# Optimization experiments

Measured on AMD Instinct MI355X. Metric: run time of the kernel, lower is better.

## Reference

```python
import jax, jax.numpy as jnp
import numpy as np

B, T_HIST, T_OUT, T_FC = 4096, 168, 48, 49
N_LABELS, F_CTL, F_FC, HID = 64, 16, 8, 32
EPS = 1e-7


def setup_inputs() -> dict:
    key = jax.random.key(0)
    ks = jax.random.split(key, 18)
    rn = lambda k, s, sc=1.0: jax.random.normal(k, s, jnp.float32) * sc
    return {
        "history": rn(ks[0], (B, T_HIST, N_LABELS)),
        "control": rn(ks[1], (B, T_OUT, F_CTL)),
        "forecasts": rn(ks[2], (B, T_FC, F_FC)),
        "h_mean": rn(ks[3], (N_LABELS,), 0.1),
        "h_var": jax.random.uniform(ks[4], (N_LABELS,), jnp.float32, 0.5, 1.5),
        "c_mean": rn(ks[5], (F_CTL,), 0.1),
        "c_var": jax.random.uniform(ks[6], (F_CTL,), jnp.float32, 0.5, 1.5),
        "f_mean": rn(ks[7], (), 0.1),
        "f_var": jax.random.uniform(ks[8], (), jnp.float32, 0.5, 1.5),
        "conv_w": rn(ks[9], (2, F_FC, 4), 0.2),   # kernel_size=2, Conv1D(4)
        "conv_b": rn(ks[10], (4,), 0.01),
        "lstm_k": rn(ks[11], (N_LABELS, 4 * HID), 0.1),
        "lstm_rk": rn(ks[12], (HID, 4 * HID), 0.1),
        "lstm_b": rn(ks[13], (4 * HID,), 0.01),
        "w1": rn(ks[14], (HID + F_CTL + 4, 64), 0.1),
        "b1": rn(ks[15], (64,), 0.01),
        "w2": rn(ks[16], (64, N_LABELS), 0.05),
        "b2": rn(ks[17], (N_LABELS,), 0.01),
    }


def _norm(x, m, v):
    # keras Normalization: (x - mean) / max(sqrt(var), eps)
    return (x - m) / jnp.maximum(jnp.sqrt(v), EPS)


def _lstm(x, h, c, k, rk, b):
    z = x @ k + h @ rk + b                      # [B, 4*HID], gate order i,f,g,o
    i, f, g, o = jnp.split(z, 4, axis=-1)
    c2 = jax.nn.sigmoid(f) * c + jax.nn.sigmoid(i) * jnp.tanh(g)
    h2 = jax.nn.sigmoid(o) * jnp.tanh(c2)
    return h2, c2


def _mlp(x1, x2, x3, w1, b1, w2, b2):
    x = jnp.concatenate([x1, x2, x3], axis=-1)  # [B, 52]
    return jax.nn.relu(x @ w1 + b1) @ w2 + b2


def reference(history, control, forecasts, h_mean, h_var, c_mean, c_var,
              f_mean, f_var, conv_w, conv_b, lstm_k, lstm_rk, lstm_b,
              w1, b1, w2, b2):
    latest = history[:, -1, :]                               # [B, N_LABELS]
    cn = _norm(control, c_mean, c_var)                       # [B, T_OUT, F_CTL]
    fn = _norm(forecasts, f_mean, f_var)                     # scalar norm
    # Conv1D(filters=4, kernel_size=2), valid padding -> [B, T_FC-1, 4]
    fc = fn[:, :-1] @ conv_w[0] + fn[:, 1:] @ conv_w[1] + conv_b

    # encoder LSTM over normalized history
    hn = _norm(history, h_mean, h_var)
    bsz = history.shape[0]
    init = (jnp.zeros((bsz, HID), hn.dtype), jnp.zeros((bsz, HID), hn.dtype))

    def enc_step(carry, x):
        h, c = carry
        return _lstm(x, h, c, lstm_k, lstm_rk, lstm_b), None

    (h, c), _ = jax.lax.scan(enc_step, init, jnp.swapaxes(hn, 0, 1))

    # pre-loop step (its prediction write is overwritten by loop i=0, but it
    # updates `latest` which feeds the loop)
    latest = latest + _mlp(h, cn[:, 0], fc[:, 0], w1, b1, w2, b2)

    t_out = control.shape[1]

    def dec_step(carry, inp):
        latest, h, c = carry
        ctl, fci = inp
        xn = _norm(latest, h_mean, h_var)
        h2, c2 = _lstm(xn, h, c, lstm_k, lstm_rk, lstm_b)
        latest2 = latest + _mlp(h2, ctl, fci, w1, b1, w2, b2)
        return (latest2, h2, c2), latest2

    xs = (jnp.swapaxes(cn, 0, 1), jnp.swapaxes(fc[:, :t_out], 0, 1))
    _, preds = jax.lax.scan(dec_step, (latest, h, c), xs)   # [T_OUT, B, N]
    return jnp.swapaxes(preds, 0, 1)                        # [B, T_OUT, N]
```

## Files before the change

### kernel.cpp

```cpp
#include <hip/hip_runtime.h>

#define EPSV 1e-7f

typedef __bf16 bf16x8 __attribute__((ext_vector_type(8)));
typedef float  f32x4  __attribute__((ext_vector_type(4)));
typedef unsigned int   u32x4 __attribute__((ext_vector_type(4)));
typedef unsigned short u16x8 __attribute__((ext_vector_type(8)));
typedef unsigned short u16x4 __attribute__((ext_vector_type(4)));

__device__ __forceinline__ unsigned short f2bf(float f) {
    unsigned int u = __float_as_uint(f);
    return (unsigned short)((u + 0x7FFFu + ((u >> 16) & 1u)) >> 16);
}
__device__ __forceinline__ float bf2f(unsigned short u) {
    return __uint_as_float(((unsigned int)u) << 16);
}
__device__ __forceinline__ void split2(float f, unsigned short& hi, unsigned short& lo) {
    hi = f2bf(f);
    lo = f2bf(f - bf2f(hi));
}
__device__ __forceinline__ void splitT(float f, unsigned short& hi, unsigned short& lo) {
    unsigned int u  = __float_as_uint(f);
    unsigned int hb = u & 0xFFFF0000u;
    float l = f - __uint_as_float(hb);
    hi = (unsigned short)(u >> 16);
    lo = (unsigned short)(__float_as_uint(l) >> 16);
}
__device__ __forceinline__ float sigf(float x) {
    return __builtin_amdgcn_rcpf(1.0f + __expf(-x));
}
__device__ __forceinline__ float tanhfast(float x) {
    float cx = fminf(fmaxf(x, -15.0f), 15.0f);
    float e = __expf(2.0f * cx);
    return (e - 1.0f) * __builtin_amdgcn_rcpf(e + 1.0f);
}
__device__ __forceinline__ float xor8(float v) {
    return __builtin_bit_cast(float, __builtin_amdgcn_update_dpp(
        0, __builtin_bit_cast(int, v), 0x128, 0xF, 0xF, true));
}

#define MFMA16(A, B, C) __builtin_amdgcn_mfma_f32_16x16x32_bf16(A, B, C, 0, 0, 0)
#define BC8(x) __builtin_bit_cast(bf16x8, x)

#define BARRIER() do {                                        \
    asm volatile("s_waitcnt lgkmcnt(0)" ::: "memory");        \
    __builtin_amdgcn_s_barrier();                             \
    __builtin_amdgcn_sched_barrier(0);                        \
} while (0)

#define HS2 72
#define MS  136
#define XS2 136

__global__ __launch_bounds__(256) void tutina_kernel(
    const float* __restrict__ history, const float* __restrict__ control,
    const float* __restrict__ forecasts,
    const float* __restrict__ h_mean, const float* __restrict__ h_var,
    const float* __restrict__ c_mean, const float* __restrict__ c_var,
    const float* __restrict__ f_mean, const float* __restrict__ f_var,
    const float* __restrict__ conv_w, const float* __restrict__ conv_b,
    const float* __restrict__ lstm_k, const float* __restrict__ lstm_rk,
    const float* __restrict__ lstm_b,
    const float* __restrict__ w1, const float* __restrict__ b1,
    const float* __restrict__ w2, const float* __restrict__ b2,
    float* __restrict__ out)
{
    __shared__ unsigned short hbuf[2][16 * HS2];
    __shared__ unsigned short xbuf[16 * XS2];
    __shared__ unsigned short mlps[16 * MS];
    __shared__ unsigned short hids[16 * MS];
    __shared__ unsigned int   fcs[48 * 64];

    const int tid  = threadIdx.x;
    const int lane = tid & 63;
    const int wid  = tid >> 6;
    const int l15  = lane & 15;
    const int l4   = lane >> 4;
    const int b0   = blockIdx.x * 16;

    for (int i = tid; i < 16 * HS2; i += 256) hbuf[0][i] = 0;
    for (int i = tid; i < 16 * MS;  i += 256) mlps[i] = 0;

    const int  uu     = l15 & 7;
    const bool lohalf = (l15 < 8);
    const int  u      = wid * 8 + uu;
    const int  jz0    = lohalf ? u      : 32 + u;
    const int  jz1    = lohalf ? 64 + u : 96 + u;
    const int  j1     = wid * 16 + l15;

    auto bfragK = [&](int kbase, int j, float& dacc, bf16x8& H, bf16x8& L) {
        u16x8 h, l;
#pragma unroll
        for (int i = 0; i < 8; i++) {
            int k = kbase + l4 * 8 + i;
            float sv = 1.0f / fmaxf(sqrtf(h_var[k]), EPSV);
            float w  = lstm_k[k * 128 + j] * sv;
            dacc += h_mean[k] * w;
            unsigned short hh, ll; split2(w, hh, ll);
            h[i] = hh; l[i] = ll;
        }
        H = BC8(h); L = BC8(l);
    };
    auto bfragP = [&](const float* W, int ldw, int kbase, int j, bf16x8& H, bf16x8& L) {
        u16x8 h, l;
#pragma unroll
        for (int i = 0; i < 8; i++) {
            int k = kbase + l4 * 8 + i;
            float w = W[k * ldw + j];
            unsigned short hh, ll; split2(w, hh, ll);
            h[i] = hh; l[i] = ll;
        }
        H = BC8(h); L = BC8(l);
    };
    auto bfragW11 = [&](int j, float& dacc, bf16x8& H, bf16x8& L) {
        u16x8 h, l;
#pragma unroll
        for (int i = 0; i < 8; i++) {
            int k = 32 + l4 * 8 + i;
            float w = 0.0f;
            if (k < 52) {
                w = w1[k * 64 + j];
                if (k < 48) {
                    float sv = 1.0f / fmaxf(sqrtf(c_var[k - 32]), EPSV);
                    w *= sv;
                    dacc += c_mean[k - 32] * w;
                }
            }
            unsigned short hh, ll; split2(w, hh, ll);
            h[i] = hh; l[i] = ll;
        }
        H = BC8(h); L = BC8(l);
    };

    bf16x8 fA0h, fA0l, fA1h, fA1l, fA2h, fA2l;
    bf16x8 fB0h, fB0l, fB1h, fB1l, fB2h, fB2l;
    bf16x8 fW10h, fW10l, fW11h, fW11l, fW20h, fW20l, fW21h, fW21l;
    float dz0 = 0.f, dz1 = 0.f, d1 = 0.f;
    bfragK(0,  jz0, dz0, fA0h, fA0l);
    bfragK(32, jz0, dz0, fA1h, fA1l);
    bfragP(lstm_rk, 128, 0, jz0, fA2h, fA2l);
    bfragK(0,  jz1, dz1, fB0h, fB0l);
    bfragK(32, jz1, dz1, fB1h, fB1l);
    bfragP(lstm_rk, 128, 0, jz1, fB2h, fB2l);
    bfragP(w1, 64, 0, j1, fW10h, fW10l);
    bfragW11(j1, d1, fW11h, fW11l);
    bfragP(w2, 64, 0,  j1, fW20h, fW20l);
    bfragP(w2, 64, 32, j1, fW21h, fW21l);

    dz0 += __shfl_xor(dz0, 16, 64); dz0 += __shfl_xor(dz0, 32, 64);
    dz1 += __shfl_xor(dz1, 16, 64); dz1 += __shfl_xor(dz1, 32, 64);
    d1  += __shfl_xor(d1, 16, 64);  d1  += __shfl_xor(d1, 32, 64);
    float pd0 = xor8(dz0), pd1 = xor8(dz1);
    const float bi_ = lstm_b[u]      - (lohalf ? dz0 : pd0);
    const float bf_ = lstm_b[32 + u] - (lohalf ? pd0 : dz0);
    const float bg_ = lstm_b[64 + u] - (lohalf ? dz1 : pd1);
    const float bo_ = lstm_b[96 + u] - (lohalf ? pd1 : dz1);
    const float b1j = b1[j1] - d1;
    const float b2j = b2[j1];

    const int r0 = l4 * 4 + (lohalf ? 0 : 2);
    const int r1 = r0 + 1;
    float c0 = 0.0f, c1 = 0.0f;

    const int rc = tid >> 2, cc = (tid & 3) * 4;

    {
        float fm  = f_mean[0];
        float fsc = 1.0f / fmaxf(sqrtf(f_var[0]), EPSV);
        for (int cell = tid; cell < 48 * 64; cell += 256) {
            int t  = cell >> 6;
            int b  = (cell >> 2) & 15;
            int uc = cell & 3;
            const float* fp = forecasts + ((size_t)(b0 + b) * 49 + t) * 8;
            float acc = conv_b[uc];
#pragma unroll
            for (int k = 0; k < 8; k++) {
                acc += (fp[k]     - fm) * fsc * conv_w[k * 4 + uc];
                acc += (fp[8 + k] - fm) * fsc * conv_w[32 + k * 4 + uc];
            }
            unsigned short hh, ll; split2(acc, hh, ll);
            fcs[cell] = ((unsigned int)hh << 16) | ll;
        }
    }

    auto lstm_gates = [&](const f32x4& a, const f32x4& b,
                          unsigned short* hw, bool write_mlp) {
        float sa0 = lohalf ? a[2] : a[0];
        float sa1 = lohalf ? a[3] : a[1];
        float sb0 = lohalf ? b[2] : b[0];
        float sb1 = lohalf ? b[3] : b[1];
        float ra0 = xor8(sa0);
        float ra1 = xor8(sa1);
        float rb0 = xor8(sb0);
        float rb1 = xor8(sb1);
        float zi0 = (lohalf ? a[0] : ra0) + bi_;
        float zi1 = (lohalf ? a[1] : ra1) + bi_;
        float zf0 = (lohalf ? ra0 : a[2]) + bf_;
        float zf1 = (lohalf ? ra1 : a[3]) + bf_;
        float zg0 = (lohalf ? b[0] : rb0) + bg_;
        float zg1 = (lohalf ? b[1] : rb1) + bg_;
        float zo0 = (lohalf ? rb0 : b[2]) + bo_;
        float zo1 = (lohalf ? rb1 : b[3]) + bo_;
        c0 = sigf(zf0) * c0 + sigf(zi0) * tanhfast(zg0);
        c1 = sigf(zf1) * c1 + sigf(zi1) * tanhfast(zg1);
        float h20 = sigf(zo0) * tanhfast(c0);
        float h21 = sigf(zo1) * tanhfast(c1);
        unsigned short bh, bl;
        splitT(h20, bh, bl);
        hw[r0 * HS2 + u]      = bh;
        hw[r0 * HS2 + 32 + u] = bl;
        if (write_mlp) { mlps[r0 * MS + u] = bh; mlps[r0 * MS + 64 + u] = bl; }
        splitT(h21, bh, bl);
        hw[r1 * HS2 + u]      = bh;
        hw[r1 * HS2 + 32 + u] = bl;
        if (write_mlp) { mlps[r1 * MS + u] = bh; mlps[r1 * MS + 64 + u] = bl; }
    };

    const float* hp = history + (size_t)(b0 + l15) * (168 * 64);
    const int o1 = l4 * 8, o2 = 32 + l4 * 8;

    auto mk_frags = [&](const f32x4& p0, const f32x4& p1, const f32x4& p2,
                        const f32x4& p3, bf16x8& A0h, bf16x8& A0l,
                        bf16x8& A1h, bf16x8& A1l) {
        u16x8 xh_, xl_;
        unsigned short hh, ll;
#pragma unroll
        for (int i = 0; i < 4; i++) { splitT(p0[i], hh, ll); xh_[i] = hh; xl_[i] = ll; }
#pragma unroll
        for (int i = 0; i < 4; i++) { splitT(p1[i], hh, ll); xh_[4+i] = hh; xl_[4+i] = ll; }
        A0h = BC8(xh_); A0l = BC8(xl_);
#pragma unroll
        for (int i = 0; i < 4; i++) { splitT(p2[i], hh, ll); xh_[i] = hh; xl_[i] = ll; }
#pragma unroll
        for (int i = 0; i < 4; i++) { splitT(p3[i], hh, ll); xh_[4+i] = hh; xl_[4+i] = ll; }
        A1h = BC8(xh_); A1l = BC8(xl_);
    };
    auto zx12 = [&](bf16x8 A0h, bf16x8 A0l, bf16x8 A1h, bf16x8 A1l,
                    f32x4& zn0, f32x4& zn1) {
        f32x4 s0 = {0.f,0.f,0.f,0.f}, s1 = {0.f,0.f,0.f,0.f};
        s0 = MFMA16(A0h, fA0h, s0);  s1 = MFMA16(A0h, fB0h, s1);
        s0 = MFMA16(A1h, fA1h, s0);  s1 = MFMA16(A1h, fB1h, s1);
        s0 = MFMA16(A0l, fA0h, s0);  s1 = MFMA16(A0l, fB0h, s1);
        s0 = MFMA16(A1l, fA1h, s0);  s1 = MFMA16(A1l, fB1h, s1);
        s0 = MFMA16(A0h, fA0l, s0);  s1 = MFMA16(A0h, fB0l, s1);
        s0 = MFMA16(A1h, fA1l, s0);  s1 = MFMA16(A1h, fB1l, s1);
        zn0 = s0; zn1 = s1;
    };

    f32x4 zx0, zx1;
    {
        f32x4 p0 = *(const f32x4*)(hp + o1), p1 = *(const f32x4*)(hp + o1 + 4);
        f32x4 p2 = *(const f32x4*)(hp + o2), p3 = *(const f32x4*)(hp + o2 + 4);
        bf16x8 A0h, A0l, A1h, A1l;
        mk_frags(p0, p1, p2, p3, A0h, A0l, A1h, A1l);
        zx12(A0h, A0l, A1h, A1l, zx0, zx1);
    }
    f32x4 vb0 = *(const f32x4*)(hp + 64 + o1), vb1 = *(const f32x4*)(hp + 64 + o1 + 4);
    f32x4 vb2 = *(const f32x4*)(hp + 64 + o2), vb3 = *(const f32x4*)(hp + 64 + o2 + 4);

    BARRIER();

    for (int t = 0; t < 168; ++t) {
        const int p = t & 1;
        const unsigned short* hr = hbuf[p];
        bf16x8 a2h = BC8(*(const u32x4*)&hr[l15 * HS2 + l4 * 8]);
        bf16x8 a2l = BC8(*(const u32x4*)&hr[l15 * HS2 + 32 + l4 * 8]);

        bf16x8 A0h, A0l, A1h, A1l;
        mk_frags(vb0, vb1, vb2, vb3, A0h, A0l, A1h, A1l);
        const float* np = hp + (size_t)((t < 166) ? t + 2 : 167) * 64;
        vb0 = *(const f32x4*)(np + o1); vb1 = *(const f32x4*)(np + o1 + 4);
        vb2 = *(const f32x4*)(np + o2); vb3 = *(const f32x4*)(np + o2 + 4);

        f32x4 zn0, zn1;
        zx12(A0h, A0l, A1h, A1l, zn0, zn1);

        f32x4 z0 = zx0, z1 = zx1;
        z0 = MFMA16(a2h, fA2h, z0);  z1 = MFMA16(a2h, fB2h, z1);
        z0 = MFMA16(a2l, fA2h, z0);  z1 = MFMA16(a2l, fB2h, z1);
        z0 = MFMA16(a2h, fA2l, z0);  z1 = MFMA16(a2h, fB2l, z1);

        lstm_gates(z0, z1, hbuf[p ^ 1], t == 167);
        BARRIER();
        zx0 = zn0; zx1 = zn1;
    }

    float lat0 = history[((size_t)(b0 + l4 * 4 + 0) * 168 + 167) * 64 + j1];
    float lat1 = history[((size_t)(b0 + l4 * 4 + 1) * 168 + 167) * 64 + j1];
    float lat2 = history[((size_t)(b0 + l4 * 4 + 2) * 168 + 167) * 64 + j1];
    float lat3 = history[((size_t)(b0 + l4 * 4 + 3) * 168 + 167) * 64 + j1];
    f32x4 creg = {0.f, 0.f, 0.f, 0.f};
    if (tid < 64)
        creg = *(const f32x4*)(control + ((size_t)(b0 + rc) * 48 + 0) * 16 + cc);

    auto stage_cn = [&](const f32x4& v) {
        if (tid < 64) {
            u16x4 oh, ol;
#pragma unroll
            for (int q = 0; q < 4; q++) {
                unsigned short hh, ll;
                splitT(v[q], hh, ll);
                oh[q] = hh; ol[q] = ll;
            }
            *(u16x4*)&mlps[rc * MS + 32 + cc]      = oh;
            *(u16x4*)&mlps[rc * MS + 64 + 32 + cc] = ol;
        }
    };
    auto stage_fc = [&](int t) {
        if (tid >= 64 && tid < 128) {
            int q = tid - 64;
            unsigned int v = fcs[t * 64 + q];
            mlps[(q >> 2) * MS + 48 + (q & 3)]      = (unsigned short)(v >> 16);
            mlps[(q >> 2) * MS + 64 + 48 + (q & 3)] = (unsigned short)(v & 0xFFFFu);
        }
    };

    auto mlp1 = [&]() {
        const int mbase = l15 * MS + l4 * 8;
        bf16x8 m0  = BC8(*(const u32x4*)&mlps[mbase]);
        bf16x8 m1  = BC8(*(const u32x4*)&mlps[mbase + 32]);
        bf16x8 m0l = BC8(*(const u32x4*)&mlps[mbase + 64]);
        bf16x8 m1l = BC8(*(const u32x4*)&mlps[mbase + 96]);
        f32x4 ha = {0.f,0.f,0.f,0.f}, hb = {0.f,0.f,0.f,0.f};
        ha = MFMA16(m0,  fW10h, ha);   hb = MFMA16(m1,  fW11h, hb);
        ha = MFMA16(m0l, fW10h, ha);   hb = MFMA16(m1l, fW11h, hb);
        ha = MFMA16(m0,  fW10l, ha);   hb = MFMA16(m1,  fW11l, hb);
        f32x4 hacc = ha + hb;
#pragma unroll
        for (int q = 0; q < 4; q++) {
            float hv = fmaxf(hacc[q] + b1j, 0.0f);
            unsigned short hh, ll;
            splitT(hv, hh, ll);
            hids[(l4 * 4 + q) * MS + j1]      = hh;
            hids[(l4 * 4 + q) * MS + 64 + j1] = ll;
        }
    };
    auto mlp2 = [&]() {
        const int mbase = l15 * MS + l4 * 8;
        bf16x8 h0  = BC8(*(const u32x4*)&hids[mbase]);
        bf16x8 h1  = BC8(*(const u32x4*)&hids[mbase + 32]);
        bf16x8 h0l = BC8(*(const u32x4*)&hids[mbase + 64]);
        bf16x8 h1l = BC8(*(const u32x4*)&hids[mbase + 96]);
        f32x4 oa = {0.f,0.f,0.f,0.f}, ob = {0.f,0.f,0.f,0.f};
        oa = MFMA16(h0,  fW20h, oa);   ob = MFMA16(h1,  fW21h, ob);
        oa = MFMA16(h0l, fW20h, oa);   ob = MFMA16(h1l, fW21h, ob);
        oa = MFMA16(h0,  fW20l, oa);   ob = MFMA16(h1,  fW21l, ob);
        f32x4 oacc = oa + ob;
        lat0 += oacc[0] + b2j;
        lat1 += oacc[1] + b2j;
        lat2 += oacc[2] + b2j;
        lat3 += oacc[3] + b2j;
    };

    stage_cn(creg);
    stage_fc(0);
    BARRIER();
    mlp1();
    BARRIER();
    mlp2();

    for (int t = 0; t < 48; ++t) {
        const int p = t & 1;
        unsigned short bh, bl;
        splitT(lat0, bh, bl);
        xbuf[(l4 * 4 + 0) * XS2 + j1] = bh; xbuf[(l4 * 4 + 0) * XS2 + 64 + j1] = bl;
        splitT(lat1, bh, bl);
        xbuf[(l4 * 4 + 1) * XS2 + j1] = bh; xbuf[(l4 * 4 + 1) * XS2 + 64 + j1] = bl;
        splitT(lat2, bh, bl);
        xbuf[(l4 * 4 + 2) * XS2 + j1] = bh; xbuf[(l4 * 4 + 2) * XS2 + 64 + j1] = bl;
        splitT(lat3, bh, bl);
        xbuf[(l4 * 4 + 3) * XS2 + j1] = bh; xbuf[(l4 * 4 + 3) * XS2 + 64 + j1] = bl;
        stage_cn(creg);
        stage_fc(t);
        int tn = (t < 47) ? t + 1 : 47;
        if (tid < 64)
            creg = *(const f32x4*)(control + ((size_t)(b0 + rc) * 48 + tn) * 16 + cc);
        BARRIER();

        const unsigned short* hr = hbuf[p];
        const int xb = l15 * XS2 + l4 * 8;
        bf16x8 a0h = BC8(*(const u32x4*)&xbuf[xb]);
        bf16x8 a1h = BC8(*(const u32x4*)&xbuf[xb + 32]);
        bf16x8 a0l = BC8(*(const u32x4*)&xbuf[xb + 64]);
        bf16x8 a1l = BC8(*(const u32x4*)&xbuf[xb + 96]);
        bf16x8 a2h = BC8(*(const u32x4*)&hr[l15 * HS2 + l4 * 8]);
        bf16x8 a2l = BC8(*(const u32x4*)&hr[l15 * HS2 + 32 + l4 * 8]);
        f32x4 z0a = {0.f,0.f,0.f,0.f}, z0b = {0.f,0.f,0.f,0.f};
        f32x4 z1a = {0.f,0.f,0.f,0.f}, z1b = {0.f,0.f,0.f,0.f};
        z0a = MFMA16(a0h, fA0h, z0a);  z1a = MFMA16(a0h, fB0h, z1a);
        z0b = MFMA16(a1h, fA1h, z0b);  z1b = MFMA16(a1h, fB1h, z1b);
        z0a = MFMA16(a2h, fA2h, z0a);  z1a = MFMA16(a2h, fB2h, z1a);
        z0b = MFMA16(a0l, fA0h, z0b);  z1b = MFMA16(a0l, fB0h, z1b);
        z0a = MFMA16(a1l, fA1h, z0a);  z1a = MFMA16(a1l, fB1h, z1a);
        z0b = MFMA16(a2l, fA2h, z0b);  z1b = MFMA16(a2l, fB2h, z1b);
        z0a = MFMA16(a0h, fA0l, z0a);  z1a = MFMA16(a0h, fB0l, z1a);
        z0b = MFMA16(a1h, fA1l, z0b);  z1b = MFMA16(a1h, fB1l, z1b);
        z0a = MFMA16(a2h, fA2l, z0a);  z1a = MFMA16(a2h, fB2l, z1a);
        f32x4 z0 = z0a + z0b, z1 = z1a + z1b;
        lstm_gates(z0, z1, hbuf[p ^ 1], true);
        BARRIER();

        mlp1();
        BARRIER();
        mlp2();

        out[((size_t)(b0 + l4 * 4 + 0) * 48 + t) * 64 + j1] = lat0;
        out[((size_t)(b0 + l4 * 4 + 1) * 48 + t) * 64 + j1] = lat1;
        out[((size_t)(b0 + l4 * 4 + 2) * 48 + t) * 64 + j1] = lat2;
        out[((size_t)(b0 + l4 * 4 + 3) * 48 + t) * 64 + j1] = lat3;
    }
}

extern "C" void kernel_launch(void* const* d_in, const int* in_sizes, int n_in,
                              void* d_out, int out_size, void* d_ws, size_t ws_size,
                              hipStream_t stream) {
    tutina_kernel<<<dim3(256), dim3(256), 0, stream>>>(
        (const float*)d_in[0],  (const float*)d_in[1],  (const float*)d_in[2],
        (const float*)d_in[3],  (const float*)d_in[4],  (const float*)d_in[5],
        (const float*)d_in[6],  (const float*)d_in[7],  (const float*)d_in[8],
        (const float*)d_in[9],  (const float*)d_in[10], (const float*)d_in[11],
        (const float*)d_in[12], (const float*)d_in[13], (const float*)d_in[14],
        (const float*)d_in[15], (const float*)d_in[16], (const float*)d_in[17],
        (float*)d_out);
}
```

Measured before the change: 186.1 us.

## Split block into recurrent and producer wave groups to overlap encoder input projection

The block grows to 512 threads as two groups of four waves. Group A does only the recurrent h@rk MFMAs and gate math, at raised priority. Group B loads history, computes the input projection one step ahead into a double-buffered shared buffer, and handles the MLP in the decoder. The aim is to take the input-projection work and global loads off the serial critical path of the 168-step recurrence. The cost is twice the waves per block, extra shared memory, and idle waves in each group during the other's phases.

```diff
diff --git a/kernel.cpp b/kernel.cpp
--- a/kernel.cpp
+++ b/kernel.cpp
@@ -51,8 +51,9 @@
 #define HS2 72
 #define MS  136
 #define XS2 136
-
-__global__ __launch_bounds__(256) void tutina_kernel(
+#define ZS3 20
+
+__global__ __launch_bounds__(512, 1) void tutina_kernel(
     const float* __restrict__ history, const float* __restrict__ control,
     const float* __restrict__ forecasts,
     const float* __restrict__ h_mean, const float* __restrict__ h_var,
@@ -66,6 +67,7 @@
     float* __restrict__ out)
 {
     __shared__ unsigned short hbuf[2][16 * HS2];
+    __shared__ float zxb[2][4][2][16 * ZS3];
     __shared__ unsigned short xbuf[16 * XS2];
     __shared__ unsigned short mlps[16 * MS];
     __shared__ unsigned short hids[16 * MS];
@@ -74,19 +76,22 @@
     const int tid  = threadIdx.x;
     const int lane = tid & 63;
     const int wid  = tid >> 6;
+    const int wa   = wid & 3;
+    const bool gA  = (wid < 4);
+    const int lt   = tid & 255;
     const int l15  = lane & 15;
     const int l4   = lane >> 4;
     const int b0   = blockIdx.x * 16;
 
-    for (int i = tid; i < 16 * HS2; i += 256) hbuf[0][i] = 0;
-    for (int i = tid; i < 16 * MS;  i += 256) mlps[i] = 0;
+    for (int i = tid; i < 16 * HS2; i += 512) hbuf[0][i] = 0;
+    for (int i = tid; i < 16 * MS;  i += 512) mlps[i] = 0;
 
     const int  uu     = l15 & 7;
     const bool lohalf = (l15 < 8);
-    const int  u      = wid * 8 + uu;
+    const int  u      = wa * 8 + uu;
     const int  jz0    = lohalf ? u      : 32 + u;
     const int  jz1    = lohalf ? 64 + u : 96 + u;
-    const int  j1     = wid * 16 + l15;
+    const int  j1     = wa * 16 + l15;
 
     auto bfragK = [&](int kbase, int j, float& dacc, bf16x8& H, bf16x8& L) {
         u16x8 h, l;
@@ -132,42 +137,51 @@
         H = BC8(h); L = BC8(l);
     };
 
-    bf16x8 fA0h, fA0l, fA1h, fA1l, fA2h, fA2l;
-    bf16x8 fB0h, fB0l, fB1h, fB1l, fB2h, fB2l;
-    bf16x8 fW10h, fW10l, fW11h, fW11l, fW20h, fW20l, fW21h, fW21l;
-    float dz0 = 0.f, dz1 = 0.f, d1 = 0.f;
+    bf16x8 fA0h, fA0l, fA1h, fA1l, fB0h, fB0l, fB1h, fB1l;
+    float dz0 = 0.f, dz1 = 0.f;
     bfragK(0,  jz0, dz0, fA0h, fA0l);
     bfragK(32, jz0, dz0, fA1h, fA1l);
-    bfragP(lstm_rk, 128, 0, jz0, fA2h, fA2l);
     bfragK(0,  jz1, dz1, fB0h, fB0l);
     bfragK(32, jz1, dz1, fB1h, fB1l);
-    bfragP(lstm_rk, 128, 0, jz1, fB2h, fB2l);
-    bfragP(w1, 64, 0, j1, fW10h, fW10l);
-    bfragW11(j1, d1, fW11h, fW11l);
-    bfragP(w2, 64, 0,  j1, fW20h, fW20l);
-    bfragP(w2, 64, 32, j1, fW21h, fW21l);
-
-    dz0 += __shfl_xor(dz0, 16, 64); dz0 += __shfl_xor(dz0, 32, 64);
-    dz1 += __shfl_xor(dz1, 16, 64); dz1 += __shfl_xor(dz1, 32, 64);
-    d1  += __shfl_xor(d1, 16, 64);  d1  += __shfl_xor(d1, 32, 64);
-    float pd0 = xor8(dz0), pd1 = xor8(dz1);
-    const float bi_ = lstm_b[u]      - (lohalf ? dz0 : pd0);
-    const float bf_ = lstm_b[32 + u] - (lohalf ? pd0 : dz0);
-    const float bg_ = lstm_b[64 + u] - (lohalf ? dz1 : pd1);
-    const float bo_ = lstm_b[96 + u] - (lohalf ? pd1 : dz1);
-    const float b1j = b1[j1] - d1;
-    const float b2j = b2[j1];
-
-    const int r0 = l4 * 4 + (lohalf ? 0 : 2);
-    const int r1 = r0 + 1;
-    float c0 = 0.0f, c1 = 0.0f;
-
-    const int rc = tid >> 2, cc = (tid & 3) * 4;
-
-    {
+
+    bf16x8 fA2h, fA2l, fB2h, fB2l;
+    float bi_ = 0.f, bf_ = 0.f, bg_ = 0.f, bo_ = 0.f;
+    if (gA) {
+        bfragP(lstm_rk, 128, 0, jz0, fA2h, fA2l);
+        bfragP(lstm_rk, 128, 0, jz1, fB2h, fB2l);
+        float z0s = dz0, z1s = dz1;
+        z0s += __shfl_xor(z0s, 16, 64); z0s += __shfl_xor(z0s, 32, 64);
+        z1s += __shfl_xor(z1s, 16, 64); z1s += __shfl_xor(z1s, 32, 64);
+        float pd0 = xor8(z0s), pd1 = xor8(z1s);
+        bi_ = lstm_b[u]      - (lohalf ? z0s : pd0);
+        bf_ = lstm_b[32 + u] - (lohalf ? pd0 : z0s);
+        bg_ = lstm_b[64 + u] - (lohalf ? z1s : pd1);
+        bo_ = lstm_b[96 + u] - (lohalf ? pd1 : z1s);
+    }
+
+    bf16x8 fW10h, fW10l, fW11h, fW11l, fW20h, fW20l, fW21h, fW21l;
+    float b1j = 0.f, b2j = 0.f;
+    float lat0 = 0.f, lat1 = 0.f, lat2 = 0.f, lat3 = 0.f;
+    f32x4 creg = {0.f, 0.f, 0.f, 0.f};
+    const int rc = lt >> 2, cc = (lt & 3) * 4;
+    if (!gA) {
+        bfragP(w1, 64, 0, j1, fW10h, fW10l);
+        float d1 = 0.f;
+        bfragW11(j1, d1, fW11h, fW11l);
+        bfragP(w2, 64, 0,  j1, fW20h, fW20l);
+        bfragP(w2, 64, 32, j1, fW21h, fW21l);
+        d1 += __shfl_xor(d1, 16, 64); d1 += __shfl_xor(d1, 32, 64);
+        b1j = b1[j1] - d1;
+        b2j = b2[j1];
+        lat0 = history[((size_t)(b0 + l4 * 4 + 0) * 168 + 167) * 64 + j1];
+        lat1 = history[((size_t)(b0 + l4 * 4 + 1) * 168 + 167) * 64 + j1];
+        lat2 = history[((size_t)(b0 + l4 * 4 + 2) * 168 + 167) * 64 + j1];
+        lat3 = history[((size_t)(b0 + l4 * 4 + 3) * 168 + 167) * 64 + j1];
+        if (lt < 64)
+            creg = *(const f32x4*)(control + ((size_t)(b0 + rc) * 48 + 0) * 16 + cc);
         float fm  = f_mean[0];
         float fsc = 1.0f / fmaxf(sqrtf(f_var[0]), EPSV);
-        for (int cell = tid; cell < 48 * 64; cell += 256) {
+        for (int cell = lt; cell < 48 * 64; cell += 256) {
             int t  = cell >> 6;
             int b  = (cell >> 2) & 15;
             int uc = cell & 3;
@@ -182,6 +196,10 @@
             fcs[cell] = ((unsigned int)hh << 16) | ll;
         }
     }
+
+    const int r0 = l4 * 4 + (lohalf ? 0 : 2);
+    const int r1 = r0 + 1;
+    float c0 = 0.0f, c1 = 0.0f;
 
     auto lstm_gates = [&](const f32x4& a, const f32x4& b,
                           unsigned short* hw, bool write_mlp) {
@@ -216,9 +234,6 @@
         if (write_mlp) { mlps[r1 * MS + u] = bh; mlps[r1 * MS + 64 + u] = bl; }
     };
 
-    const float* hp = history + (size_t)(b0 + l15) * (168 * 64);
-    const int o1 = l4 * 8, o2 = 32 + l4 * 8;
-
     auto mk_frags = [&](const f32x4& p0, const f32x4& p1, const f32x4& p2,
                         const f32x4& p3, bf16x8& A0h, bf16x8& A0l,
                         bf16x8& A1h, bf16x8& A1l) {
@@ -247,54 +262,53 @@
         zn0 = s0; zn1 = s1;
     };
 
-    f32x4 zx0, zx1;
-    {
+    const float* hp = history + (size_t)(b0 + l15) * (168 * 64);
+    const int o1 = l4 * 8, o2 = 32 + l4 * 8;
+    const int zoff = l15 * ZS3 + l4 * 4;
+    f32x4 vb0, vb1, vb2, vb3;
+    if (!gA) {
         f32x4 p0 = *(const f32x4*)(hp + o1), p1 = *(const f32x4*)(hp + o1 + 4);
         f32x4 p2 = *(const f32x4*)(hp + o2), p3 = *(const f32x4*)(hp + o2 + 4);
         bf16x8 A0h, A0l, A1h, A1l;
         mk_frags(p0, p1, p2, p3, A0h, A0l, A1h, A1l);
-        zx12(A0h, A0l, A1h, A1l, zx0, zx1);
+        f32x4 zn0, zn1;
+        zx12(A0h, A0l, A1h, A1l, zn0, zn1);
+        *(f32x4*)&zxb[0][wa][0][zoff] = zn0;
+        *(f32x4*)&zxb[0][wa][1][zoff] = zn1;
+        vb0 = *(const f32x4*)(hp + 64 + o1); vb1 = *(const f32x4*)(hp + 64 + o1 + 4);
+        vb2 = *(const f32x4*)(hp + 64 + o2); vb3 = *(const f32x4*)(hp + 64 + o2 + 4);
     }
-    f32x4 vb0 = *(const f32x4*)(hp + 64 + o1), vb1 = *(const f32x4*)(hp + 64 + o1 + 4);
-    f32x4 vb2 = *(const f32x4*)(hp + 64 + o2), vb3 = *(const f32x4*)(hp + 64 + o2 + 4);
-
+    if (gA) __builtin_amdgcn_s_setprio(1);
     BARRIER();
 
     for (int t = 0; t < 168; ++t) {
         const int p = t & 1;
-        const unsigned short* hr = hbuf[p];
-        bf16x8 a2h = BC8(*(const u32x4*)&hr[l15 * HS2 + l4 * 8]);
-        bf16x8 a2l = BC8(*(const u32x4*)&hr[l15 * HS2 + 32 + l4 * 8]);
-
-        bf16x8 A0h, A0l, A1h, A1l;
-        mk_frags(vb0, vb1, vb2, vb3, A0h, A0l, A1h, A1l);
-        const float* np = hp + (size_t)((t < 166) ? t + 2 : 167) * 64;
-        vb0 = *(const f32x4*)(np + o1); vb1 = *(const f32x4*)(np + o1 + 4);
-        vb2 = *(const f32x4*)(np + o2); vb3 = *(const f32x4*)(np + o2 + 4);
-
-        f32x4 zn0, zn1;
-        zx12(A0h, A0l, A1h, A1l, zn0, zn1);
-
-        f32x4 z0 = zx0, z1 = zx1;
-        z0 = MFMA16(a2h, fA2h, z0);  z1 = MFMA16(a2h, fB2h, z1);
-        z0 = MFMA16(a2l, fA2h, z0);  z1 = MFMA16(a2l, fB2h, z1);
-        z0 = MFMA16(a2h, fA2l, z0);  z1 = MFMA16(a2h, fB2l, z1);
-
-        lstm_gates(z0, z1, hbuf[p ^ 1], t == 167);
+        if (gA) {
+            const unsigned short* hr = hbuf[p];
+            bf16x8 a2h = BC8(*(const u32x4*)&hr[l15 * HS2 + l4 * 8]);
+            bf16x8 a2l = BC8(*(const u32x4*)&hr[l15 * HS2 + 32 + l4 * 8]);
+            f32x4 z0 = *(const f32x4*)&zxb[p][wa][0][zoff];
+            f32x4 z1 = *(const f32x4*)&zxb[p][wa][1][zoff];
+            z0 = MFMA16(a2h, fA2h, z0);  z1 = MFMA16(a2h, fB2h, z1);
+            z0 = MFMA16(a2l, fA2h, z0);  z1 = MFMA16(a2l, fB2h, z1);
+            z0 = MFMA16(a2h, fA2l, z0);  z1 = MFMA16(a2h, fB2l, z1);
+            lstm_gates(z0, z1, hbuf[p ^ 1], t == 167);
+        } else {
+            bf16x8 A0h, A0l, A1h, A1l;
+            mk_frags(vb0, vb1, vb2, vb3, A0h, A0l, A1h, A1l);
+            const float* np = hp + (size_t)((t < 166) ? t + 2 : 167) * 64;
+            vb0 = *(const f32x4*)(np + o1); vb1 = *(const f32x4*)(np + o1 + 4);
+            vb2 = *(const f32x4*)(np + o2); vb3 = *(const f32x4*)(np + o2 + 4);
+            f32x4 zn0, zn1;
+            zx12(A0h, A0l, A1h, A1l, zn0, zn1);
+            *(f32x4*)&zxb[p ^ 1][wa][0][zoff] = zn0;
+            *(f32x4*)&zxb[p ^ 1][wa][1][zoff] = zn1;
+        }
         BARRIER();
-        zx0 = zn0; zx1 = zn1;
     }
 
-    float lat0 = history[((size_t)(b0 + l4 * 4 + 0) * 168 + 167) * 64 + j1];
-    float lat1 = history[((size_t)(b0 + l4 * 4 + 1) * 168 + 167) * 64 + j1];
-    float lat2 = history[((size_t)(b0 + l4 * 4 + 2) * 168 + 167) * 64 + j1];
-    float lat3 = history[((size_t)(b0 + l4 * 4 + 3) * 168 + 167) * 64 + j1];
-    f32x4 creg = {0.f, 0.f, 0.f, 0.f};
-    if (tid < 64)
-        creg = *(const f32x4*)(control + ((size_t)(b0 + rc) * 48 + 0) * 16 + cc);
-
     auto stage_cn = [&](const f32x4& v) {
-        if (tid < 64) {
+        if (lt < 64) {
             u16x4 oh, ol;
 #pragma unroll
             for (int q = 0; q < 4; q++) {
@@ -307,14 +321,13 @@
         }
     };
     auto stage_fc = [&](int t) {
-        if (tid >= 64 && tid < 128) {
-            int q = tid - 64;
+        if (lt >= 64 && lt < 128) {
+            int q = lt - 64;
             unsigned int v = fcs[t * 64 + q];
             mlps[(q >> 2) * MS + 48 + (q & 3)]      = (unsigned short)(v >> 16);
             mlps[(q >> 2) * MS + 64 + 48 + (q & 3)] = (unsigned short)(v & 0xFFFFu);
         }
     };
-
     auto mlp1 = [&]() {
         const int mbase = l15 * MS + l4 * 8;
         bf16x8 m0  = BC8(*(const u32x4*)&mlps[mbase]);
@@ -352,69 +365,74 @@
         lat3 += oacc[3] + b2j;
     };
 
-    stage_cn(creg);
-    stage_fc(0);
+    if (!gA) { stage_cn(creg); stage_fc(0); }
     BARRIER();
-    mlp1();
+    if (!gA) mlp1();
     BARRIER();
-    mlp2();
+    if (!gA) mlp2();
 
     for (int t = 0; t < 48; ++t) {
         const int p = t & 1;
-        unsigned short bh, bl;
-        splitT(lat0, bh, bl);
-        xbuf[(l4 * 4 + 0) * XS2 + j1] = bh; xbuf[(l4 * 4 + 0) * XS2 + 64 + j1] = bl;
-        splitT(lat1, bh, bl);
-        xbuf[(l4 * 4 + 1) * XS2 + j1] = bh; xbuf[(l4 * 4 + 1) * XS2 + 64 + j1] = bl;
-        splitT(lat2, bh, bl);
-        xbuf[(l4 * 4 + 2) * XS2 + j1] = bh; xbuf[(l4 * 4 + 2) * XS2 + 64 + j1] = bl;
-        splitT(lat3, bh, bl);
-        xbuf[(l4 * 4 + 3) * XS2 + j1] = bh; xbuf[(l4 * 4 + 3) * XS2 + 64 + j1] = bl;
-        stage_cn(creg);
-        stage_fc(t);
-        int tn = (t < 47) ? t + 1 : 47;
-        if (tid < 64)
-            creg = *(const f32x4*)(control + ((size_t)(b0 + rc) * 48 + tn) * 16 + cc);
+        if (!gA) {
+            unsigned short bh, bl;
+            splitT(lat0, bh, bl);
+            xbuf[(l4 * 4 + 0) * XS2 + j1] = bh; xbuf[(l4 * 4 + 0) * XS2 + 64 + j1] = bl;
+            splitT(lat1, bh, bl);
+            xbuf[(l4 * 4 + 1) * XS2 + j1] = bh; xbuf[(l4 * 4 + 1) * XS2 + 64 + j1] = bl;
+            splitT(lat2, bh, bl);
+            xbuf[(l4 * 4 + 2) * XS2 + j1] = bh; xbuf[(l4 * 4 + 2) * XS2 + 64 + j1] = bl;
+            splitT(lat3, bh, bl);
+            xbuf[(l4 * 4 + 3) * XS2 + j1] = bh; xbuf[(l4 * 4 + 3) * XS2 + 64 + j1] = bl;
+            stage_cn(creg);
+            stage_fc(t);
+            int tn = (t < 47) ? t + 1 : 47;
+            if (lt < 64)
+                creg = *(const f32x4*)(control + ((size_t)(b0 + rc) * 48 + tn) * 16 + cc);
+        }
         BARRIER();
 
-        const unsigned short* hr = hbuf[p];
-        const int xb = l15 * XS2 + l4 * 8;
-        bf16x8 a0h = BC8(*(const u32x4*)&xbuf[xb]);
-        bf16x8 a1h = BC8(*(const u32x4*)&xbuf[xb + 32]);
-        bf16x8 a0l = BC8(*(const u32x4*)&xbuf[xb + 64]);
-        bf16x8 a1l = BC8(*(const u32x4*)&xbuf[xb + 96]);
-        bf16x8 a2h = BC8(*(const u32x4*)&hr[l15 * HS2 + l4 * 8]);
-        bf16x8 a2l = BC8(*(const u32x4*)&hr[l15 * HS2 + 32 + l4 * 8]);
-        f32x4 z0a = {0.f,0.f,0.f,0.f}, z0b = {0.f,0.f,0.f,0.f};
-        f32x4 z1a = {0.f,0.f,0.f,0.f}, z1b = {0.f,0.f,0.f,0.f};
-        z0a = MFMA16(a0h, fA0h, z0a);  z1a = MFMA16(a0h, fB0h, z1a);
-        z0b = MFMA16(a1h, fA1h, z0b);  z1b = MFMA16(a1h, fB1h, z1b);
-        z0a = MFMA16(a2h, fA2h, z0a);  z1a = MFMA16(a2h, fB2h, z1a);
-        z0b = MFMA16(a0l, fA0h, z0b);  z1b = MFMA16(a0l, fB0h, z1b);
-        z0a = MFMA16(a1l, fA1h, z0a);  z1a = MFMA16(a1l, fB1h, z1a);
-        z0b = MFMA16(a2l, fA2h, z0b);  z1b = MFMA16(a2l, fB2h, z1b);
-        z0a = MFMA16(a0h, fA0l, z0a);  z1a = MFMA16(a0h, fB0l, z1a);
-        z0b = MFMA16(a1h, fA1l, z0b);  z1b = MFMA16(a1h, fB1l, z1b);
-        z0a = MFMA16(a2h, fA2l, z0a);  z1a = MFMA16(a2h, fB2l, z1a);
-        f32x4 z0 = z0a + z0b, z1 = z1a + z1b;
-        lstm_gates(z0, z1, hbuf[p ^ 1], true);
+        if (gA) {
+            const unsigned short* hr = hbuf[p];
+            const int xb = l15 * XS2 + l4 * 8;
+            bf16x8 a0h = BC8(*(const u32x4*)&xbuf[xb]);
+            bf16x8 a1h = BC8(*(const u32x4*)&xbuf[xb + 32]);
+            bf16x8 a0l = BC8(*(const u32x4*)&xbuf[xb + 64]);
+            bf16x8 a1l = BC8(*(const u32x4*)&xbuf[xb + 96]);
+            bf16x8 a2h = BC8(*(const u32x4*)&hr[l15 * HS2 + l4 * 8]);
+            bf16x8 a2l = BC8(*(const u32x4*)&hr[l15 * HS2 + 32 + l4 * 8]);
+            f32x4 z0a = {0.f,0.f,0.f,0.f}, z0b = {0.f,0.f,0.f,0.f};
+            f32x4 z1a = {0.f,0.f,0.f,0.f}, z1b = {0.f,0.f,0.f,0.f};
+            z0a = MFMA16(a0h, fA0h, z0a);  z1a = MFMA16(a0h, fB0h, z1a);
+            z0b = MFMA16(a1h, fA1h, z0b);  z1b = MFMA16(a1h, fB1h, z1b);
+            z0a = MFMA16(a2h, fA2h, z0a);  z1a = MFMA16(a2h, fB2h, z1a);
+            z0b = MFMA16(a0l, fA0h, z0b);  z1b = MFMA16(a0l, fB0h, z1b);
+            z0a = MFMA16(a1l, fA1h, z0a);  z1a = MFMA16(a1l, fB1h, z1a);
+            z0b = MFMA16(a2l, fA2h, z0b);  z1b = MFMA16(a2l, fB2h, z1b);
+            z0a = MFMA16(a0h, fA0l, z0a);  z1a = MFMA16(a0h, fB0l, z1a);
+            z0b = MFMA16(a1h, fA1l, z0b);  z1b = MFMA16(a1h, fB1l, z1b);
+            z0a = MFMA16(a2h, fA2l, z0a);  z1a = MFMA16(a2h, fB2l, z1a);
+            f32x4 z0 = z0a + z0b, z1 = z1a + z1b;
+            lstm_gates(z0, z1, hbuf[p ^ 1], true);
+        }
         BARRIER();
 
-        mlp1();
+        if (!gA) mlp1();
         BARRIER();
-        mlp2();
-
-        out[((size_t)(b0 + l4 * 4 + 0) * 48 + t) * 64 + j1] = lat0;
-        out[((size_t)(b0 + l4 * 4 + 1) * 48 + t) * 64 + j1] = lat1;
-        out[((size_t)(b0 + l4 * 4 + 2) * 48 + t) * 64 + j1] = lat2;
-        out[((size_t)(b0 + l4 * 4 + 3) * 48 + t) * 64 + j1] = lat3;
+
+        if (!gA) {
+            mlp2();
+            out[((size_t)(b0 + l4 * 4 + 0) * 48 + t) * 64 + j1] = lat0;
+            out[((size_t)(b0 + l4 * 4 + 1) * 48 + t) * 64 + j1] = lat1;
+            out[((size_t)(b0 + l4 * 4 + 2) * 48 + t) * 64 + j1] = lat2;
+            out[((size_t)(b0 + l4 * 4 + 3) * 48 + t) * 64 + j1] = lat3;
+        }
     }
 }
 
 extern "C" void kernel_launch(void* const* d_in, const int* in_sizes, int n_in,
                               void* d_out, int out_size, void* d_ws, size_t ws_size,
                               hipStream_t stream) {
-    tutina_kernel<<<dim3(256), dim3(256), 0, stream>>>(
+    tutina_kernel<<<dim3(256), dim3(512), 0, stream>>>(
         (const float*)d_in[0],  (const float*)d_in[1],  (const float*)d_in[2],
         (const float*)d_in[3],  (const float*)d_in[4],  (const float*)d_in[5],
         (const float*)d_in[6],  (const float*)d_in[7],  (const float*)d_in[8],
```

After: 170.0 us. 8.7% less time.
